# Optimization experiments

Measured on AMD Instinct MI355X. Metric: run time of the kernel, lower is better.

The kernel has to match this reference:

```python
import jax, jax.numpy as jnp
import numpy as np

T, B, E, H, L = 512, 64, 300, 800, 3  # seq, batch, embed, per-layer hidden, layers


def setup_inputs() -> dict:
    key = jax.random.key(0)
    ks = jax.random.split(key, 8)
    s = 0.05
    return {
        "sent": jax.random.normal(ks[0], (T, B, E), jnp.float32),
        "lengths": jax.random.randint(ks[1], (B,), 1, T + 1),
        "W0": jax.random.normal(ks[2], (E, 3 * H), jnp.float32) * s,
        "b0": jnp.zeros((3 * H,), jnp.float32),
        "W1": jax.random.normal(ks[3], (H, 3 * H), jnp.float32) * s,
        "b1": jnp.zeros((3 * H,), jnp.float32),
        "W2": jax.random.normal(ks[4], (H, 3 * H), jnp.float32) * s,
        "b2": jnp.zeros((3 * H,), jnp.float32),
    }


def _fo_pool(f, z):
    # c_t = f_t * z_t + (1 - f_t) * c_{t-1}, c_0 = 0  (ForgetMult)
    # linear recurrence c_t = a_t * c_{t-1} + b_t with a = 1-f, b = f*z
    a = 1.0 - f
    b = f * z
    def comb(c1, c2):
        a1, b1 = c1
        a2, b2 = c2
        return (a2 * a1, a2 * b1 + b2)
    _, C = jax.lax.associative_scan(comb, (a, b), axis=0)
    return C  # [T,B,H]; initial state is zero so C is exactly the pooled state


def _qrnn_layer(x, W, b):
    g = jnp.einsum('tbe,eh->tbh', x, W) + b  # [T,B,3H]
    z, f, o = jnp.split(g, 3, axis=-1)
    C = _fo_pool(jax.nn.sigmoid(f), jnp.tanh(z))
    return jax.nn.sigmoid(o) * C, C[-1]


def reference(sent, lengths, W0, b0, W1, b1, W2, b2):
    h = sent
    finals = []
    for W, bb in ((W0, b0), (W1, b1), (W2, b2)):
        h, c_last = _qrnn_layer(h, W, bb)
        finals.append(c_last)
    hn = jnp.stack(finals, axis=0)            # [L,B,H]
    out = jnp.transpose(hn, (1, 0, 2)).reshape(B, L * H)  # [B, L*H]
    return out
```

## Files before the change

### kernel.cpp

```cpp
#include <hip/hip_runtime.h>
#include <hip/hip_bf16.h>
#include <cstdint>
#include <cstddef>


typedef __bf16 bf16_t;
typedef __bf16 bf16x8 __attribute__((ext_vector_type(8)));
typedef float f32x4 __attribute__((ext_vector_type(4)));

#define T_C 128
#define NCHUNK 4
#define BATCH 64
#define EMB 300
#define HID 800
#define LDH 832
#define MC (T_C * BATCH)

__device__ __forceinline__ float fast_sigmoid(float x) {
  return 1.0f / (1.0f + __expf(-x));
}
__device__ __forceinline__ float fast_tanh(float x) {
  return 2.0f / (1.0f + __expf(-2.0f * x)) - 1.0f;
}
__device__ __forceinline__ float b2f(uint32_t u) {
  union { uint32_t i; float f; } x;
  x.i = u << 16;
  return x.f;
}

__global__ __launch_bounds__(256) void cast_reorder_a0(
    const float* __restrict__ X, bf16_t* __restrict__ Y) {
  int idx = blockIdx.x * 256 + threadIdx.x;
  if (idx >= 32768 * 320) return;
  int r = idx / 320, col = idx - r * 320;
  const int cc = r >> 13, b = (r >> 7) & 63, t = r & 127;
  const int src = (cc * 128 + t) * 64 + b;
  float v = (col < EMB) ? X[(size_t)src * EMB + col] : 0.0f;
  Y[idx] = (bf16_t)v;
}

__global__ __launch_bounds__(256) void transpose_cast_w(
    const float* __restrict__ W0, const float* __restrict__ W1,
    const float* __restrict__ W2, bf16_t* __restrict__ M0,
    bf16_t* __restrict__ M1, bf16_t* __restrict__ Z2) {
  const int z = blockIdx.z;
  const float* W = z == 0 ? W0 : (z == 1 ? W1 : W2);
  bf16_t* Wt = z == 0 ? M0 : (z == 1 ? M1 : Z2);
  const int K = z == 0 ? 300 : 800;
  const int Kpad = z == 0 ? 320 : 832;
  const int Npad = (z < 2) ? 2496 : 1664;
  const int i = blockIdx.x, j = blockIdx.y;
  if (i * 32 >= Npad || j * 32 >= Kpad) return;
  __shared__ float tile[32][33];
  const int tx = threadIdx.x & 31, ty = threadIdx.x >> 5;
#pragma unroll
  for (int r = 0; r < 32; r += 8) {
    const int k = j * 32 + ty + r;
    const int n = i * 32 + tx;
    int h, src;
    if (z < 2) {
      const int jt = n / 192, rr = n - jt * 192;
      if (rr < 128) {
        h = jt * 64 + (rr >> 1);
        src = (rr & 1) * 800 + h;
      } else {
        h = jt * 64 + (rr - 128);
        src = 1600 + h;
      }
    } else {
      h = n >> 1;
      src = (n & 1) * 800 + h;
    }
    const bool valid = (k < K) && (h < 800);
    tile[ty + r][tx] = valid ? W[(size_t)k * 2400 + src] : 0.0f;
  }
  __syncthreads();
#pragma unroll
  for (int r = 0; r < 32; r += 8) {
    const int n = i * 32 + ty + r, k = j * 32 + tx;
    if (n < Npad && k < Kpad)
      Wt[(size_t)n * Kpad + k] = (bf16_t)tile[tx][ty + r];
  }
}

__device__ __forceinline__ void stage16(const bf16_t* gp, bf16_t* lp) {
  __builtin_amdgcn_global_load_lds((__attribute__((address_space(1))) void*)gp,
                                   (__attribute__((address_space(3))) void*)lp,
                                   16, 0, 0);
}

template <int NTF, int ETS>
__device__ __forceinline__ void gemm_tile_to_lds(
    const bf16_t* __restrict__ A, const bf16_t* __restrict__ Bt,
    bf16_t* __restrict__ S, int K, int mBase, int nBase) {
  bf16_t* As = S;
  bf16_t* Bs = S + 8192;
  const int tid = threadIdx.x;
  const int wave = tid >> 6, lane = tid & 63;
  const int wm = wave >> 1, wn = wave & 1;
  const int srow = tid >> 3;
  const int scolSw = ((tid & 7) ^ (srow & 7)) * 8;
  const size_t aBase = (size_t)(mBase + srow) * K + scolSw;
  const size_t bBase = (size_t)(nBase + srow) * K + scolSw;
  const int ldsOff = tid * 8;

  f32x4 acc[4][NTF];
#pragma unroll
  for (int mt = 0; mt < 4; ++mt)
#pragma unroll
    for (int nt = 0; nt < NTF; ++nt) {
      f32x4 zz = {0.0f, 0.0f, 0.0f, 0.0f};
      acc[mt][nt] = zz;
    }

  const int fr = lane & 15, fq = lane >> 4;
  const int x0 = fr & 7;
  const int ckEl0 = (fq ^ x0) * 8;
  const int ckEl1 = ((4 + fq) ^ x0) * 8;

  for (int k0 = 0; k0 < K; k0 += 64) {
#pragma unroll
    for (int p = 0; p < 4; ++p)
      stage16(A + aBase + (size_t)(32 * p) * K + k0, &As[ldsOff + p * 2048]);
#pragma unroll
    for (int p = 0; p < NTF; ++p)
      stage16(Bt + bBase + (size_t)(32 * p) * K + k0, &Bs[ldsOff + p * 2048]);
    __syncthreads();
#pragma unroll
    for (int kh = 0; kh < 2; ++kh) {
      const int ck = kh ? ckEl1 : ckEl0;
      bf16x8 af[4], bfv[NTF];
#pragma unroll
      for (int mt = 0; mt < 4; ++mt)
        af[mt] = *(const bf16x8*)&As[(wm * 64 + mt * 16 + fr) * 64 + ck];
#pragma unroll
      for (int nt = 0; nt < NTF; ++nt)
        bfv[nt] = *(const bf16x8*)&Bs[(wn * (16 * NTF) + nt * 16 + fr) * 64 + ck];
#pragma unroll
      for (int mt = 0; mt < 4; ++mt)
#pragma unroll
        for (int nt = 0; nt < NTF; ++nt)
          acc[mt][nt] = __builtin_amdgcn_mfma_f32_16x16x32_bf16(
              af[mt], bfv[nt], acc[mt][nt], 0, 0, 0);
    }
    __syncthreads();
  }
  bf16_t* Et = S;
#pragma unroll
  for (int mt = 0; mt < 4; ++mt)
#pragma unroll
    for (int nt = 0; nt < NTF; ++nt)
#pragma unroll
      for (int r = 0; r < 4; ++r)
        Et[(wm * 64 + mt * 16 + fq * 4 + r) * ETS + wn * (16 * NTF) + nt * 16 +
           fr] = (bf16_t)acc[mt][nt][r];
  __syncthreads();
}

__device__ __forceinline__ void scan_h_body(
    const bf16_t* __restrict__ A, const bf16_t* __restrict__ Wm,
    const float* __restrict__ bias, bf16_t* __restrict__ Hout,
    float* __restrict__ carry, float* __restrict__ outC, int K, int outOff,
    int first, int last, int b, int ntile, bf16_t* S, float (*SA)[64],
    float (*SB)[64], float (*SC)[64]) {
  gemm_tile_to_lds<6, 196>(A, Wm, S, K, b * 128, ntile * 192);

  const uint32_t* Ep = (const uint32_t*)S;
  const int tid = threadIdx.x;
  const int hl = tid & 63, s = tid >> 6;
  const int h = ntile * 64 + hl;
  const bool hOK = (h < HID);
  const int hb = hOK ? h : 0;
  const float bz = bias[hb], bf = bias[hb + 800], bo = bias[hb + 1600];

  float av[32], bv[32];
  float Aa = 1.0f, Bb = 0.0f;
#pragma unroll
  for (int q = 0; q < 32; ++q) {
    const int t = s * 32 + q;
    const uint32_t v = Ep[t * 98 + hl];
    const float zv = fast_tanh(b2f(v & 0xffffu) + bz);
    const float fv = fast_sigmoid(b2f(v >> 16) + bf);
    av[q] = 1.0f - fv;
    bv[q] = fv * zv;
    Aa *= av[q];
    Bb = fmaf(av[q], Bb, bv[q]);
  }
  SA[s][hl] = Aa;
  SB[s][hl] = Bb;
  __syncthreads();
  if (tid < 64) {
    const int h2 = ntile * 64 + tid;
    const bool ok2 = (h2 < HID);
    float c = (first || !ok2) ? 0.0f : carry[b * HID + h2];
#pragma unroll
    for (int ss = 0; ss < 4; ++ss) {
      SC[ss][tid] = c;
      c = fmaf(SA[ss][tid], c, SB[ss][tid]);
    }
    if (ok2) {
      carry[b * HID + h2] = c;
      if (last) outC[b * 2400 + outOff + h2] = c;
    }
  }
  __syncthreads();
  float c = SC[s][hl];
#pragma unroll
  for (int q = 0; q < 32; ++q) {
    const int t = s * 32 + q;
    c = fmaf(av[q], c, bv[q]);
    const float o = fast_sigmoid((float)S[t * 196 + 128 + hl] + bo);
    Hout[(size_t)(b * 128 + t) * LDH + h] =
        hOK ? (bf16_t)(o * c) : (bf16_t)0.0f;
  }
}

__device__ __forceinline__ void scan_c_body(
    const bf16_t* __restrict__ A, const bf16_t* __restrict__ Wzf,
    const float* __restrict__ bias, float* __restrict__ carry,
    float* __restrict__ outC, int K, int outOff, int first, int last, int b,
    int ntile, bf16_t* S, float (*SA)[64], float (*SB)[64]) {
  gemm_tile_to_lds<4, 140>(A, Wzf, S, K, b * 128, ntile * 128);

  const uint32_t* Ep = (const uint32_t*)S;
  const int tid = threadIdx.x;
  const int hl = tid & 63, s = tid >> 6;
  const int h = ntile * 64 + hl;
  const int hb = (h < HID) ? h : 0;
  const float bz = bias[hb], bf = bias[hb + 800];

  float Aa = 1.0f, Bb = 0.0f;
#pragma unroll
  for (int q = 0; q < 32; ++q) {
    const int t = s * 32 + q;
    const uint32_t v = Ep[t * 70 + hl];
    const float zv = fast_tanh(b2f(v & 0xffffu) + bz);
    const float fv = fast_sigmoid(b2f(v >> 16) + bf);
    const float a = 1.0f - fv;
    Aa *= a;
    Bb = fmaf(a, Bb, fv * zv);
  }
  SA[s][hl] = Aa;
  SB[s][hl] = Bb;
  __syncthreads();
  if (tid < 64) {
    const int h2 = ntile * 64 + tid;
    const bool ok2 = (h2 < HID);
    float c = (first || !ok2) ? 0.0f : carry[b * HID + h2];
#pragma unroll
    for (int ss = 0; ss < 4; ++ss) c = fmaf(SA[ss][tid], c, SB[ss][tid]);
    if (ok2) {
      carry[b * HID + h2] = c;
      if (last) outC[b * 2400 + outOff + h2] = c;
    }
  }
}

__device__ __forceinline__ void block_tile(int& b, int& ntile) {
  const int nT = 13;
  const int L = blockIdx.y * nT + blockIdx.x;
  const int xcd = L & 7, j = L >> 3;
  b = xcd * 8 + j / nT;
  ntile = j % nT;
}

struct Role {
  const bf16_t* A;
  const bf16_t* W;
  const float* bias;
  bf16_t* Hout;
  float* carry;
  int K;
  int outOff;
  int type;
  int first;
  int last;
};

__global__ __launch_bounds__(256, 3) void gemm_scan_multi(
    Role r0, Role r1, Role r2, float* __restrict__ outC) {
  __shared__ __align__(16) bf16_t S[25088];
  __shared__ float SA[4][64], SB[4][64], SC[4][64];
  int b, ntile;
  block_tile(b, ntile);
  const Role r = blockIdx.z == 0 ? r0 : (blockIdx.z == 1 ? r1 : r2);
  if (r.type == 1)
    scan_h_body(r.A, r.W, r.bias, r.Hout, r.carry, outC, r.K, r.outOff,
                r.first, r.last, b, ntile, S, SA, SB, SC);
  else
    scan_c_body(r.A, r.W, r.bias, r.carry, outC, r.K, r.outOff, r.first,
                r.last, b, ntile, S, SA, SB);
}

extern "C" void kernel_launch(void* const* d_in, const int* in_sizes, int n_in,
                              void* d_out, int out_size, void* d_ws, size_t ws_size,
                              hipStream_t stream) {
  const float* sent = (const float*)d_in[0];
  const float* W0 = (const float*)d_in[2];
  const float* b0 = (const float*)d_in[3];
  const float* W1 = (const float*)d_in[4];
  const float* b1 = (const float*)d_in[5];
  const float* W2 = (const float*)d_in[6];
  const float* b2 = (const float*)d_in[7];
  float* out = (float*)d_out;

  char* ws = (char*)d_ws;
  size_t off = 0;
  auto alloc = [&](size_t bytes) {
    void* p = ws + off;
    off += (bytes + 255) & ~(size_t)255;
    return p;
  };
  bf16_t* Wm0 = (bf16_t*)alloc((size_t)2496 * 320 * 2);
  bf16_t* Wm1 = (bf16_t*)alloc((size_t)2496 * 832 * 2);
  bf16_t* Wzf2 = (bf16_t*)alloc((size_t)1664 * 832 * 2);
  bf16_t* A0 = (bf16_t*)alloc((size_t)32768 * 320 * 2);
  bf16_t* H0buf[2], *H1buf[2];
  H0buf[0] = (bf16_t*)alloc((size_t)MC * LDH * 2);
  H0buf[1] = (bf16_t*)alloc((size_t)MC * LDH * 2);
  H1buf[0] = (bf16_t*)alloc((size_t)MC * LDH * 2);
  H1buf[1] = (bf16_t*)alloc((size_t)MC * LDH * 2);
  float* car0 = (float*)alloc((size_t)BATCH * HID * 4);
  float* car1 = (float*)alloc((size_t)BATCH * HID * 4);
  float* car2 = (float*)alloc((size_t)BATCH * HID * 4);
  if (off > ws_size) return;

  cast_reorder_a0<<<(32768 * 320 + 255) / 256, 256, 0, stream>>>(sent, A0);
  transpose_cast_w<<<dim3(78, 26, 3), 256, 0, stream>>>(W0, W1, W2, Wm0, Wm1,
                                                        Wzf2);

  auto mkL0 = [&](int c) -> Role {
    return Role{A0 + (size_t)c * MC * 320, Wm0, b0, H0buf[c & 1], car0,
                320, 0, 1, c == 0, c == NCHUNK - 1};
  };
  auto mkL1 = [&](int c) -> Role {
    return Role{H0buf[c & 1], Wm1, b1, H1buf[c & 1], car1,
                832, 800, 1, c == 0, c == NCHUNK - 1};
  };
  auto mkL2 = [&](int c) -> Role {
    return Role{H1buf[c & 1], Wzf2, b2, nullptr, car2,
                832, 1600, 2, c == 0, c == NCHUNK - 1};
  };

  {
    Role a = mkL0(0);
    gemm_scan_multi<<<dim3(13, 64, 1), 256, 0, stream>>>(a, a, a, out);
  }
  {
    Role a = mkL1(0), b_ = mkL0(1);
    gemm_scan_multi<<<dim3(13, 64, 2), 256, 0, stream>>>(a, b_, b_, out);
  }
  for (int c = 1; c <= 2; ++c) {
    Role a = mkL1(c), b_ = mkL2(c - 1), d = mkL0(c + 1);
    gemm_scan_multi<<<dim3(13, 64, 3), 256, 0, stream>>>(a, b_, d, out);
  }
  {
    Role a = mkL1(3), b_ = mkL2(2);
    gemm_scan_multi<<<dim3(13, 64, 2), 256, 0, stream>>>(a, b_, b_, out);
  }
  {
    Role a = mkL2(3);
    gemm_scan_multi<<<dim3(13, 64, 1), 256, 0, stream>>>(a, a, a, out);
  }
}
```

Measured before the change: 495.8 us.

## Fold input cast into weight prep and overlap later chunks with layer-0 GEMM

The separate input cast/reorder kernel is removed. Chunk 0 of the input is converted inside the weight-prep kernel as an extra grid slice. Chunks 1-3 are converted by extra z-slices of the first gemm_scan launch, so that conversion runs alongside the layer-0 chunk-0 compute. The cast is also vectorized to 8 elements per thread with 16-byte loads and stores. This drops a kernel launch and hides the cast bandwidth behind compute, at the cost of a larger first launch and an extra Role argument.

After: 465.4 us. 1.07x faster.

```diff
diff --git a/kernel.cpp b/kernel.cpp
--- a/kernel.cpp
+++ b/kernel.cpp
@@ -15,6 +15,7 @@
 #define HID 800
 #define LDH 832
 #define MC (T_C * BATCH)
+#define CAST_OPS (MC * 320 / 8)
 
 __device__ __forceinline__ float fast_sigmoid(float x) {
   return 1.0f / (1.0f + __expf(-x));
@@ -28,22 +29,42 @@
   return x.f;
 }
 
-__global__ __launch_bounds__(256) void cast_reorder_a0(
-    const float* __restrict__ X, bf16_t* __restrict__ Y) {
-  int idx = blockIdx.x * 256 + threadIdx.x;
-  if (idx >= 32768 * 320) return;
-  int r = idx / 320, col = idx - r * 320;
-  const int cc = r >> 13, b = (r >> 7) & 63, t = r & 127;
-  const int src = (cc * 128 + t) * 64 + b;
-  float v = (col < EMB) ? X[(size_t)src * EMB + col] : 0.0f;
-  Y[idx] = (bf16_t)v;
-}
-
-__global__ __launch_bounds__(256) void transpose_cast_w(
+__device__ __forceinline__ void cast_op(const float* __restrict__ X,
+                                        bf16_t* __restrict__ Y, int cc,
+                                        int id) {
+  const int rr = id / 40, cb = id - rr * 40;
+  const int b = rr >> 7, t = rr & 127;
+  const float* src = X + (size_t)((cc * 128 + t) * 64 + b) * EMB + cb * 8;
+  bf16x8 w;
+  if (cb < 37) {
+    const f32x4 v0 = *(const f32x4*)src;
+    const f32x4 v1 = *(const f32x4*)(src + 4);
+#pragma unroll
+    for (int e = 0; e < 4; ++e) {
+      w[e] = (bf16_t)v0[e];
+      w[e + 4] = (bf16_t)v1[e];
+    }
+  } else {
+#pragma unroll
+    for (int e = 0; e < 8; ++e) {
+      const int col = cb * 8 + e;
+      w[e] = (bf16_t)((col < EMB) ? src[e] : 0.0f);
+    }
+  }
+  *(bf16x8*)&Y[((size_t)cc * MC + rr) * 320 + cb * 8] = w;
+}
+
+__global__ __launch_bounds__(256) void prep_all(
     const float* __restrict__ W0, const float* __restrict__ W1,
     const float* __restrict__ W2, bf16_t* __restrict__ M0,
-    bf16_t* __restrict__ M1, bf16_t* __restrict__ Z2) {
+    bf16_t* __restrict__ M1, bf16_t* __restrict__ Z2,
+    const float* __restrict__ sent, bf16_t* __restrict__ A0) {
   const int z = blockIdx.z;
+  if (z == 3) {
+    const int id = (blockIdx.y * gridDim.x + blockIdx.x) * 256 + threadIdx.x;
+    if (id < CAST_OPS) cast_op(sent, A0, 0, id);
+    return;
+  }
   const float* W = z == 0 ? W0 : (z == 1 ? W1 : W2);
   bf16_t* Wt = z == 0 ? M0 : (z == 1 ? M1 : Z2);
   const int K = z == 0 ? 300 : 800;
@@ -278,12 +299,22 @@
 };
 
 __global__ __launch_bounds__(256, 3) void gemm_scan_multi(
-    Role r0, Role r1, Role r2, float* __restrict__ outC) {
+    Role r0, Role r1, Role r2, Role r3, float* __restrict__ outC) {
   __shared__ __align__(16) bf16_t S[25088];
   __shared__ float SA[4][64], SB[4][64], SC[4][64];
+  const Role r = blockIdx.z == 0
+                     ? r0
+                     : (blockIdx.z == 1 ? r1 : (blockIdx.z == 2 ? r2 : r3));
+  if (r.type == 3) {
+    int id = (blockIdx.y * gridDim.x + blockIdx.x) * 256 + threadIdx.x;
+    const int stride = gridDim.x * gridDim.y * 256;
+#pragma unroll
+    for (int it = 0; it < 2; ++it, id += stride)
+      if (id < CAST_OPS) cast_op((const float*)r.A, r.Hout, r.outOff, id);
+    return;
+  }
   int b, ntile;
   block_tile(b, ntile);
-  const Role r = blockIdx.z == 0 ? r0 : (blockIdx.z == 1 ? r1 : r2);
   if (r.type == 1)
     scan_h_body(r.A, r.W, r.bias, r.Hout, r.carry, outC, r.K, r.outOff,
                 r.first, r.last, b, ntile, S, SA, SB, SC);
@@ -325,9 +356,8 @@
   float* car2 = (float*)alloc((size_t)BATCH * HID * 4);
   if (off > ws_size) return;
 
-  cast_reorder_a0<<<(32768 * 320 + 255) / 256, 256, 0, stream>>>(sent, A0);
-  transpose_cast_w<<<dim3(78, 26, 3), 256, 0, stream>>>(W0, W1, W2, Wm0, Wm1,
-                                                        Wzf2);
+  prep_all<<<dim3(78, 26, 4), 256, 0, stream>>>(W0, W1, W2, Wm0, Wm1, Wzf2,
+                                                sent, A0);
 
   auto mkL0 = [&](int c) -> Role {
     return Role{A0 + (size_t)c * MC * 320, Wm0, b0, H0buf[c & 1], car0,
@@ -341,25 +371,29 @@
     return Role{H1buf[c & 1], Wzf2, b2, nullptr, car2,
                 832, 1600, 2, c == 0, c == NCHUNK - 1};
   };
+  auto mkCast = [&](int c) -> Role {
+    return Role{(const bf16_t*)sent, nullptr, nullptr, A0, nullptr,
+                0, c, 3, 0, 0};
+  };
 
   {
-    Role a = mkL0(0);
-    gemm_scan_multi<<<dim3(13, 64, 1), 256, 0, stream>>>(a, a, a, out);
+    Role a = mkL0(0), c1 = mkCast(1), c2 = mkCast(2), c3 = mkCast(3);
+    gemm_scan_multi<<<dim3(13, 64, 4), 256, 0, stream>>>(a, c1, c2, c3, out);
   }
   {
     Role a = mkL1(0), b_ = mkL0(1);
-    gemm_scan_multi<<<dim3(13, 64, 2), 256, 0, stream>>>(a, b_, b_, out);
+    gemm_scan_multi<<<dim3(13, 64, 2), 256, 0, stream>>>(a, b_, b_, b_, out);
   }
   for (int c = 1; c <= 2; ++c) {
     Role a = mkL1(c), b_ = mkL2(c - 1), d = mkL0(c + 1);
-    gemm_scan_multi<<<dim3(13, 64, 3), 256, 0, stream>>>(a, b_, d, out);
+    gemm_scan_multi<<<dim3(13, 64, 3), 256, 0, stream>>>(a, b_, d, d, out);
   }
   {
     Role a = mkL1(3), b_ = mkL2(2);
-    gemm_scan_multi<<<dim3(13, 64, 2), 256, 0, stream>>>(a, b_, b_, out);
+    gemm_scan_multi<<<dim3(13, 64, 2), 256, 0, stream>>>(a, b_, b_, b_, out);
   }
   {
     Role a = mkL2(3);
-    gemm_scan_multi<<<dim3(13, 64, 1), 256, 0, stream>>>(a, a, a, out);
-  }
-}
+    gemm_scan_multi<<<dim3(13, 64, 1), 256, 0, stream>>>(a, a, a, a, out);
+  }
+}
```
